# Kernel optimization log

Hardware: AMD Instinct MI355X
Metric: run time of the kernel (lower is better)

## Reference

```python
import jax, jax.numpy as jnp
import numpy as np

VOCAB = 50257
D_MODEL = 4096
RANK = 32
ALPHA = 16.0
SCALING = ALPHA / RANK


def setup_inputs() -> dict:
    key = jax.random.key(0)
    k_ids, k_q, k_a, k_b = jax.random.split(key, 4)
    input_ids = jax.random.randint(k_ids, (4, 4096), 0, VOCAB, dtype=jnp.int32)
    # int8-quantized base embedding table and its dequant scale
    w_base_q = jax.random.randint(k_q, (VOCAB, D_MODEL), -127, 128, dtype=jnp.int8)
    w_scale = jnp.array([0.01], dtype=jnp.float32)
    # LoRA adapters: A kaiming-uniform-like, B near-zero
    bound = 1.0 / np.sqrt(RANK)
    adapter_A = jax.random.uniform(k_a, (VOCAB, RANK), minval=-bound, maxval=bound, dtype=jnp.float32)
    adapter_B = jax.random.normal(k_b, (RANK, D_MODEL), dtype=jnp.float32) * 1e-4
    return {
        "input_ids": input_ids,
        "w_base_q": w_base_q,
        "w_scale": w_scale,
        "adapter_A": adapter_A,
        "adapter_B": adapter_B,
    }


def reference(input_ids, w_base_q, w_scale, adapter_A, adapter_B) -> jnp.ndarray:
    # Gather int8 rows and dequantize with scalar scale -> [B, S, D]
    w_base = w_base_q[input_ids].astype(jnp.float32) * w_scale[0]
    # LoRA: gather low-rank rows [B, S, r], project through B [r, D]
    a_out = adapter_A[input_ids]
    lora = jnp.einsum("bsr,rd->bsd", a_out, adapter_B) * SCALING
    return w_base + lora
```

## Files before the change

### kernel.cpp

```cpp
#include <hip/hip_runtime.h>
#include <stdint.h>

constexpr int D_MODEL = 4096;
constexpr int RANK = 32;
constexpr int TPB = 16;
constexpr float SCALING = 0.5f;

__global__ __launch_bounds__(256, 4)
void lora_embed_kernel(const int* __restrict__ ids,
                       const int* __restrict__ wq,
                       const float* __restrict__ scale,
                       const float* __restrict__ A,
                       const float* __restrict__ Bm,
                       float* __restrict__ out)
{
    __shared__ float sA[RANK][TPB];
    __shared__ int sTok[TPB];

    const int tid = threadIdx.x;
    const int t0 = blockIdx.x * TPB;

    if (tid < TPB) sTok[tid] = ids[t0 + tid];
    __syncthreads();

    {
        int i = tid;
        int t = i >> 5, r = i & 31;
        sA[r][t] = A[(int64_t)sTok[t] * RANK + r] * SCALING;
        i += 256;
        t = i >> 5; r = i & 31;
        sA[r][t] = A[(int64_t)sTok[t] * RANK + r] * SCALING;
    }
    __syncthreads();

    const float s = scale[0];

    int tok[TPB];
    #pragma unroll
    for (int t = 0; t < TPB; ++t) tok[t] = sTok[t];

    const float4* sA4 = (const float4*)&sA[0][0];

    for (int p = 0; p < 4; ++p) {
        const int d = p * 1024 + (tid << 2);

        float4 acc[TPB];
        #pragma unroll
        for (int t = 0; t < TPB; ++t) acc[t] = make_float4(0.f, 0.f, 0.f, 0.f);

        #pragma unroll 8
        for (int r = 0; r < RANK; ++r) {
            const float4 b = *(const float4*)(Bm + r * D_MODEL + d);
            float a[TPB];
            *(float4*)&a[0]  = sA4[r * 4 + 0];
            *(float4*)&a[4]  = sA4[r * 4 + 1];
            *(float4*)&a[8]  = sA4[r * 4 + 2];
            *(float4*)&a[12] = sA4[r * 4 + 3];
            #pragma unroll
            for (int t = 0; t < TPB; ++t) {
                acc[t].x += a[t] * b.x;
                acc[t].y += a[t] * b.y;
                acc[t].z += a[t] * b.z;
                acc[t].w += a[t] * b.w;
            }
        }

        #pragma unroll
        for (int t = 0; t < TPB; ++t) {
            const int4 w = *(const int4*)(wq + (int64_t)tok[t] * D_MODEL + d);
            float4 o;
            o.x = (float)w.x * s + acc[t].x;
            o.y = (float)w.y * s + acc[t].y;
            o.z = (float)w.z * s + acc[t].z;
            o.w = (float)w.w * s + acc[t].w;
            *(float4*)(out + (int64_t)(t0 + t) * D_MODEL + d) = o;
        }
    }
}

extern "C" void kernel_launch(void* const* d_in, const int* in_sizes, int n_in,
                              void* d_out, int out_size, void* d_ws, size_t ws_size,
                              hipStream_t stream)
{
    const int*   ids   = (const int*)d_in[0];
    const int*   wq    = (const int*)d_in[1];
    const float* scale = (const float*)d_in[2];
    const float* A     = (const float*)d_in[3];
    const float* Bm    = (const float*)d_in[4];
    float* out = (float*)d_out;

    const int n_tok  = in_sizes[0];
    const int blocks = n_tok / TPB;
    lora_embed_kernel<<<blocks, 256, 0, stream>>>(ids, wq, scale, A, Bm, out);
}
```

Before: 1.054 ms.

## Prefetch base rows before LoRA FMA loop, shrink token tile, use nontemporal stores

The token tile per block drops from 16 to 8 and the block from 256 to 128 threads, so there are twice as many blocks and eight column passes instead of four. In each pass the quantized base-table rows are now loaded before the rank-32 FMA loop, so their gather latency overlaps the LoRA arithmetic instead of trailing it. Output writes use nontemporal stores to avoid polluting the cache with streaming data. The cost is that each B row is reloaded for fewer tokens, which roughly doubles B traffic, and more registers stay live to hold the prefetched rows.

```diff
diff --git a/kernel.cpp b/kernel.cpp
--- a/kernel.cpp
+++ b/kernel.cpp
@@ -2,11 +2,15 @@
 #include <stdint.h>
 
 constexpr int D_MODEL = 4096;
-constexpr int RANK = 32;
-constexpr int TPB = 16;
+constexpr int RANK    = 32;
+constexpr int TPB     = 8;
+constexpr int THREADS = 128;
+constexpr int PASSES  = D_MODEL / (THREADS * 4);
 constexpr float SCALING = 0.5f;
 
-__global__ __launch_bounds__(256, 4)
+typedef float f32x4 __attribute__((ext_vector_type(4)));
+
+__global__ __launch_bounds__(THREADS, 4)
 void lora_embed_kernel(const int* __restrict__ ids,
                        const int* __restrict__ wq,
                        const float* __restrict__ scale,
@@ -15,10 +19,10 @@
                        float* __restrict__ out)
 {
     __shared__ float sA[RANK][TPB];
-    __shared__ int sTok[TPB];
+    __shared__ int   sTok[TPB];
 
     const int tid = threadIdx.x;
-    const int t0 = blockIdx.x * TPB;
+    const int t0  = blockIdx.x * TPB;
 
     if (tid < TPB) sTok[tid] = ids[t0 + tid];
     __syncthreads();
@@ -27,53 +31,56 @@
         int i = tid;
         int t = i >> 5, r = i & 31;
         sA[r][t] = A[(int64_t)sTok[t] * RANK + r] * SCALING;
-        i += 256;
-        t = i >> 5; r = i & 31;
+        i += THREADS; t = i >> 5; r = i & 31;
         sA[r][t] = A[(int64_t)sTok[t] * RANK + r] * SCALING;
     }
     __syncthreads();
 
     const float s = scale[0];
 
-    int tok[TPB];
+    int wrow[TPB];
     #pragma unroll
-    for (int t = 0; t < TPB; ++t) tok[t] = sTok[t];
+    for (int t = 0; t < TPB; ++t) wrow[t] = sTok[t] * D_MODEL;
 
-    const float4* sA4 = (const float4*)&sA[0][0];
+    const f32x4* sA4 = (const f32x4*)&sA[0][0];
 
-    for (int p = 0; p < 4; ++p) {
-        const int d = p * 1024 + (tid << 2);
+    for (int p = 0; p < PASSES; ++p) {
+        const int d = p * (THREADS * 4) + (tid << 2);
 
-        float4 acc[TPB];
+        int4 w[TPB];
         #pragma unroll
-        for (int t = 0; t < TPB; ++t) acc[t] = make_float4(0.f, 0.f, 0.f, 0.f);
+        for (int t = 0; t < TPB; ++t)
+            w[t] = *(const int4*)(wq + wrow[t] + d);
 
-        #pragma unroll 8
+        f32x4 acc[TPB];
+        const f32x4 zero = {0.f, 0.f, 0.f, 0.f};
+        #pragma unroll
+        for (int t = 0; t < TPB; ++t) acc[t] = zero;
+
+        const float* bp = Bm + d;
+        #pragma unroll 4
         for (int r = 0; r < RANK; ++r) {
-            const float4 b = *(const float4*)(Bm + r * D_MODEL + d);
-            float a[TPB];
-            *(float4*)&a[0]  = sA4[r * 4 + 0];
-            *(float4*)&a[4]  = sA4[r * 4 + 1];
-            *(float4*)&a[8]  = sA4[r * 4 + 2];
-            *(float4*)&a[12] = sA4[r * 4 + 3];
-            #pragma unroll
-            for (int t = 0; t < TPB; ++t) {
-                acc[t].x += a[t] * b.x;
-                acc[t].y += a[t] * b.y;
-                acc[t].z += a[t] * b.z;
-                acc[t].w += a[t] * b.w;
-            }
+            const f32x4 b   = *(const f32x4*)(bp + r * D_MODEL);
+            const f32x4 alo = sA4[r * 2 + 0];
+            const f32x4 ahi = sA4[r * 2 + 1];
+            acc[0] += alo.x * b;
+            acc[1] += alo.y * b;
+            acc[2] += alo.z * b;
+            acc[3] += alo.w * b;
+            acc[4] += ahi.x * b;
+            acc[5] += ahi.y * b;
+            acc[6] += ahi.z * b;
+            acc[7] += ahi.w * b;
         }
 
         #pragma unroll
         for (int t = 0; t < TPB; ++t) {
-            const int4 w = *(const int4*)(wq + (int64_t)tok[t] * D_MODEL + d);
-            float4 o;
-            o.x = (float)w.x * s + acc[t].x;
-            o.y = (float)w.y * s + acc[t].y;
-            o.z = (float)w.z * s + acc[t].z;
-            o.w = (float)w.w * s + acc[t].w;
-            *(float4*)(out + (int64_t)(t0 + t) * D_MODEL + d) = o;
+            f32x4 o;
+            o.x = (float)w[t].x * s + acc[t].x;
+            o.y = (float)w[t].y * s + acc[t].y;
+            o.z = (float)w[t].z * s + acc[t].z;
+            o.w = (float)w[t].w * s + acc[t].w;
+            __builtin_nontemporal_store(o, (f32x4*)(out + (int64_t)(t0 + t) * D_MODEL + d));
         }
     }
 }
@@ -91,5 +98,5 @@
 
     const int n_tok  = in_sizes[0];
     const int blocks = n_tok / TPB;
-    lora_embed_kernel<<<blocks, 256, 0, stream>>>(ids, wq, scale, A, Bm, out);
+    lora_embed_kernel<<<blocks, THREADS, 0, stream>>>(ids, wq, scale, A, Bm, out);
 }
```

Result: slower. 1.107 ms (+5.0%).
